# Kernel optimization log

Hardware: AMD Instinct MI355X
Metric: run time of the kernel (lower is better)

Reference implementation:

```python
import jax, jax.numpy as jnp
import numpy as np

EPS = 1e-05


def setup_inputs() -> dict:
    key = jax.random.key(0)
    k1, k2, k3 = jax.random.split(key, 3)
    B, S, D = 8, 4096, 1024  # batch, row(seq_len), col(d_model)
    x = jax.random.normal(k1, (B, S, D), dtype=jnp.float32)
    alpha = jnp.ones((D,), dtype=jnp.float32)
    beta = jnp.zeros((D,), dtype=jnp.float32)
    return {"x": x, "alpha": alpha, "beta": beta}


def reference(x, alpha, beta):
    # Faithful translation of LayerNorm_v2.forward, including its quirks:
    #  - statistics computed ONLY from batch element 0 (loop over x_t[0])
    #  - nonstandard running-mean recurrence: mean = (mean + data) / i
    #  - var accumulates (data - mean_i)^2 against the *updated* running mean
    #  - Bessel-style divide by (col - 1)
    # x: [B, S, D]; stats are per-row (per S), computed by streaming over D.
    B, S, D = x.shape
    data = x[0].T  # [D, S] -> loop iterates over the D (col) dimension

    def step(carry, d):
        mean, var, i = carry
        mean = (mean + d) / i          # quirky running mean
        var = var + jnp.square(d - mean)
        return (mean, var, i + 1.0), None

    init = (jnp.zeros((S,), x.dtype), jnp.zeros((S,), x.dtype),
            jnp.asarray(1.0, x.dtype))
    (mean, var, _), _ = jax.lax.scan(step, init, data)
    var = var / (D - 1)
    mean = mean[:, None]  # [S, 1]
    var = var[:, None]    # [S, 1]
    # broadcast stats from batch 0 across the whole batch, per-feature affine
    return alpha * (x - mean) / jnp.sqrt(var + EPS) + beta
```

## Files before the change

kernel.cpp:

```cpp
#include <hip/hip_runtime.h>
#include <math.h>

#define BB 8
#define SS 4096
#define DD 1024
#define EPSF 1e-5f

typedef float f32x4 __attribute__((ext_vector_type(4)));

__global__ __launch_bounds__(64) void stats_kernel(
    const float* __restrict__ x,
    float* __restrict__ mean_out,
    float* __restrict__ rstd_out)
{
    const int row = blockIdx.x;
    const int L   = threadIdx.x;
    const float4* __restrict__ rowp =
        reinterpret_cast<const float4*>(x) + (size_t)row * (DD / 4);

    const float4 a0 = rowp[4 * L + 0];
    const float4 a1 = rowp[4 * L + 1];
    const float4 a2 = rowp[4 * L + 2];
    const float4 a3 = rowp[4 * L + 3];
    const float d[16] = { a0.x, a0.y, a0.z, a0.w,  a1.x, a1.y, a1.z, a1.w,
                          a2.x, a2.y, a2.z, a2.w,  a3.x, a3.y, a3.z, a3.w };

    float m = 0.0f;
    if (L > 0) {
        const float4 p0 = rowp[4 * L - 2];
        const float4 p1 = rowp[4 * L - 1];
        const float jf = (float)(16 * L);
        float acc = p0.z;
        acc = fmaf(acc, __builtin_amdgcn_rcpf(jf - 5.0f), p0.w);
        acc = fmaf(acc, __builtin_amdgcn_rcpf(jf - 4.0f), p1.x);
        acc = fmaf(acc, __builtin_amdgcn_rcpf(jf - 3.0f), p1.y);
        acc = fmaf(acc, __builtin_amdgcn_rcpf(jf - 2.0f), p1.z);
        acc = fmaf(acc, __builtin_amdgcn_rcpf(jf - 1.0f), p1.w);
        m = acc * __builtin_amdgcn_rcpf(jf);
    }

    float var = 0.0f;
    const float base = (float)(16 * L);
#pragma unroll
    for (int t = 0; t < 16; ++t) {
        const float rk = __builtin_amdgcn_rcpf(base + (float)(t + 1));
        m = (m + d[t]) * rk;
        const float df = d[t] - m;
        var = fmaf(df, df, var);
    }

#pragma unroll
    for (int off = 32; off >= 1; off >>= 1) var += __shfl_down(var, off, 64);
    const float mean_final = __shfl(m, 63, 64);

    if (L == 0) {
        mean_out[row] = mean_final;
        rstd_out[row] = rsqrtf(var * (1.0f / 1023.0f) + EPSF);
    }
}

__global__ __launch_bounds__(256) void norm_kernel(
    const float* __restrict__ x,
    const float* __restrict__ alpha,
    const float* __restrict__ beta,
    const float* __restrict__ meanp,
    const float* __restrict__ rstdp,
    float* __restrict__ out)
{
    const int tid  = threadIdx.x;
    const int brow = blockIdx.x;
    const int s    = brow & (SS - 1);

    const float m = meanp[s];
    const float r = rstdp[s];

    const size_t i4 = (size_t)brow * 256 + tid;
    const f32x4 xv = __builtin_nontemporal_load(
        reinterpret_cast<const f32x4*>(x) + i4);
    const float4 av = reinterpret_cast<const float4*>(alpha)[tid];
    const float4 bv = reinterpret_cast<const float4*>(beta)[tid];

    f32x4 o;
    o.x = fmaf(av.x * (xv.x - m), r, bv.x);
    o.y = fmaf(av.y * (xv.y - m), r, bv.y);
    o.z = fmaf(av.z * (xv.z - m), r, bv.z);
    o.w = fmaf(av.w * (xv.w - m), r, bv.w);
    __builtin_nontemporal_store(o, reinterpret_cast<f32x4*>(out) + i4);
}

extern "C" void kernel_launch(void* const* d_in, const int* in_sizes, int n_in,
                              void* d_out, int out_size, void* d_ws, size_t ws_size,
                              hipStream_t stream) {
    (void)in_sizes; (void)n_in; (void)out_size; (void)ws_size;
    const float* x     = (const float*)d_in[0];
    const float* alpha = (const float*)d_in[1];
    const float* beta  = (const float*)d_in[2];
    float* out     = (float*)d_out;
    float* mean_ws = (float*)d_ws;
    float* rstd_ws = mean_ws + SS;

    hipLaunchKernelGGL(stats_kernel, dim3(SS), dim3(64), 0, stream,
                       x, mean_ws, rstd_ws);
    hipLaunchKernelGGL(norm_kernel, dim3(BB * SS), dim3(256), 0, stream,
                       x, alpha, beta, mean_ws, rstd_ws, out);
}
```

Before: 226.7 us.

## Fuse batch-0 normalization into stats kernel; persistent multi-row norm for rest

The stats kernel now also writes normalized output for batch 0, since it already holds those rows in registers, using an xor butterfly so every lane has the variance. That saves re-reading batch 0 in the second kernel. The norm kernel now covers only batches 1-7 with 2048 blocks, each handling 14 rows and prefetching the next row's data. This reduces block count and launch overhead but makes the grid depend on exact row counts (2048*14 = 7*4096).

```diff
diff --git a/kernel.cpp b/kernel.cpp
--- a/kernel.cpp
+++ b/kernel.cpp
@@ -8,8 +8,11 @@
 
 typedef float f32x4 __attribute__((ext_vector_type(4)));
 
-__global__ __launch_bounds__(64) void stats_kernel(
+__global__ __launch_bounds__(64) void stats_norm0_kernel(
     const float* __restrict__ x,
+    const float* __restrict__ alpha,
+    const float* __restrict__ beta,
+    float* __restrict__ out,
     float* __restrict__ mean_out,
     float* __restrict__ rstd_out)
 {
@@ -50,16 +53,35 @@
     }
 
 #pragma unroll
-    for (int off = 32; off >= 1; off >>= 1) var += __shfl_down(var, off, 64);
+    for (int off = 32; off >= 1; off >>= 1) var += __shfl_xor(var, off, 64);
     const float mean_final = __shfl(m, 63, 64);
+    const float r = rsqrtf(var * (1.0f / 1023.0f) + EPSF);
 
     if (L == 0) {
         mean_out[row] = mean_final;
-        rstd_out[row] = rsqrtf(var * (1.0f / 1023.0f) + EPSF);
+        rstd_out[row] = r;
+    }
+
+    const float4* __restrict__ alpha4 = reinterpret_cast<const float4*>(alpha);
+    const float4* __restrict__ beta4  = reinterpret_cast<const float4*>(beta);
+    f32x4* __restrict__ outp = reinterpret_cast<f32x4*>(out) + (size_t)row * (DD / 4);
+#pragma unroll
+    for (int q = 0; q < 4; ++q) {
+        const float4 av = alpha4[4 * L + q];
+        const float4 bv = beta4[4 * L + q];
+        f32x4 o;
+        o.x = fmaf(av.x * (d[4 * q + 0] - mean_final), r, bv.x);
+        o.y = fmaf(av.y * (d[4 * q + 1] - mean_final), r, bv.y);
+        o.z = fmaf(av.z * (d[4 * q + 2] - mean_final), r, bv.z);
+        o.w = fmaf(av.w * (d[4 * q + 3] - mean_final), r, bv.w);
+        __builtin_nontemporal_store(o, outp + 4 * L + q);
     }
 }
 
-__global__ __launch_bounds__(256) void norm_kernel(
+#define NBLK 2048
+#define RPB  14
+
+__global__ __launch_bounds__(256) void norm_rest_kernel(
     const float* __restrict__ x,
     const float* __restrict__ alpha,
     const float* __restrict__ beta,
@@ -67,25 +89,44 @@
     const float* __restrict__ rstdp,
     float* __restrict__ out)
 {
-    const int tid  = threadIdx.x;
-    const int brow = blockIdx.x;
-    const int s    = brow & (SS - 1);
-
-    const float m = meanp[s];
-    const float r = rstdp[s];
-
-    const size_t i4 = (size_t)brow * 256 + tid;
-    const f32x4 xv = __builtin_nontemporal_load(
-        reinterpret_cast<const f32x4*>(x) + i4);
+    const int tid = threadIdx.x;
     const float4 av = reinterpret_cast<const float4*>(alpha)[tid];
     const float4 bv = reinterpret_cast<const float4*>(beta)[tid];
 
+    const f32x4* __restrict__ xp = reinterpret_cast<const f32x4*>(x);
+    f32x4* __restrict__ op       = reinterpret_cast<f32x4*>(out);
+
+    const int row0 = SS + blockIdx.x * RPB;
+    size_t i4 = (size_t)row0 * (DD / 4) + tid;
+
+    f32x4 cur = __builtin_nontemporal_load(xp + i4);
+    float m = meanp[row0 & (SS - 1)];
+    float r = rstdp[row0 & (SS - 1)];
+
+#pragma unroll
+    for (int j = 0; j < RPB - 1; ++j) {
+        const int  rown = row0 + j + 1;
+        const size_t i4n = i4 + (DD / 4);
+        const f32x4 nxt = __builtin_nontemporal_load(xp + i4n);
+        const float mn  = meanp[rown & (SS - 1)];
+        const float rn  = rstdp[rown & (SS - 1)];
+
+        f32x4 o;
+        o.x = fmaf(av.x * (cur.x - m), r, bv.x);
+        o.y = fmaf(av.y * (cur.y - m), r, bv.y);
+        o.z = fmaf(av.z * (cur.z - m), r, bv.z);
+        o.w = fmaf(av.w * (cur.w - m), r, bv.w);
+        __builtin_nontemporal_store(o, op + i4);
+
+        cur = nxt; m = mn; r = rn; i4 = i4n;
+    }
+
     f32x4 o;
-    o.x = fmaf(av.x * (xv.x - m), r, bv.x);
-    o.y = fmaf(av.y * (xv.y - m), r, bv.y);
-    o.z = fmaf(av.z * (xv.z - m), r, bv.z);
-    o.w = fmaf(av.w * (xv.w - m), r, bv.w);
-    __builtin_nontemporal_store(o, reinterpret_cast<f32x4*>(out) + i4);
+    o.x = fmaf(av.x * (cur.x - m), r, bv.x);
+    o.y = fmaf(av.y * (cur.y - m), r, bv.y);
+    o.z = fmaf(av.z * (cur.z - m), r, bv.z);
+    o.w = fmaf(av.w * (cur.w - m), r, bv.w);
+    __builtin_nontemporal_store(o, op + i4);
 }
 
 extern "C" void kernel_launch(void* const* d_in, const int* in_sizes, int n_in,
@@ -99,8 +140,8 @@
     float* mean_ws = (float*)d_ws;
     float* rstd_ws = mean_ws + SS;
 
-    hipLaunchKernelGGL(stats_kernel, dim3(SS), dim3(64), 0, stream,
-                       x, mean_ws, rstd_ws);
-    hipLaunchKernelGGL(norm_kernel, dim3(BB * SS), dim3(256), 0, stream,
+    hipLaunchKernelGGL(stats_norm0_kernel, dim3(SS), dim3(64), 0, stream,
+                       x, alpha, beta, out, mean_ws, rstd_ws);
+    hipLaunchKernelGGL(norm_rest_kernel, dim3(NBLK), dim3(256), 0, stream,
                        x, alpha, beta, mean_ws, rstd_ws, out);
 }
```

Measured after the change: 234.7 us. +3.6%, slower.

## Fuse stats and normalization into one kernel with per-row batch loop

Applied to the files above, without the earlier changes.

Merges the statistics kernel and the normalization kernel into a single kernel where each 64-thread block computes row stats from batch 0 and then normalizes that row across all 8 batches. Batch 0 data is reused from registers, and the remaining batches are streamed with a one-ahead prefetch. This removes the second launch, the workspace round-trip, and one full reread of batch 0. The cost is fewer independent waves for the bulk streaming work, which may lower memory-level parallelism.

```diff
diff --git a/kernel.cpp b/kernel.cpp
--- a/kernel.cpp
+++ b/kernel.cpp
@@ -8,15 +8,20 @@
 
 typedef float f32x4 __attribute__((ext_vector_type(4)));
 
-__global__ __launch_bounds__(64) void stats_kernel(
+__global__ __launch_bounds__(64) void fused_ln_kernel(
     const float* __restrict__ x,
-    float* __restrict__ mean_out,
-    float* __restrict__ rstd_out)
+    const float* __restrict__ alpha,
+    const float* __restrict__ beta,
+    float* __restrict__ out)
 {
     const int row = blockIdx.x;
     const int L   = threadIdx.x;
-    const float4* __restrict__ rowp =
-        reinterpret_cast<const float4*>(x) + (size_t)row * (DD / 4);
+    const size_t row4   = (size_t)row * (DD / 4);
+    const size_t batch4 = (size_t)SS * (DD / 4);
+
+    const f32x4*  __restrict__ xp   = reinterpret_cast<const f32x4*>(x);
+    f32x4*        __restrict__ op   = reinterpret_cast<f32x4*>(out);
+    const float4* __restrict__ rowp = reinterpret_cast<const float4*>(x) + row4;
 
     const float4 a0 = rowp[4 * L + 0];
     const float4 a1 = rowp[4 * L + 1];
@@ -25,10 +30,26 @@
     const float d[16] = { a0.x, a0.y, a0.z, a0.w,  a1.x, a1.y, a1.z, a1.w,
                           a2.x, a2.y, a2.z, a2.w,  a3.x, a3.y, a3.z, a3.w };
 
+    float4 p0 = {0,0,0,0}, p1 = {0,0,0,0};
+    if (L > 0) {
+        p0 = rowp[4 * L - 2];
+        p1 = rowp[4 * L - 1];
+    }
+
+    const size_t b1 = batch4 + row4;
+    f32x4 cur[4];
+#pragma unroll
+    for (int q = 0; q < 4; ++q)
+        cur[q] = __builtin_nontemporal_load(xp + b1 + 4 * L + q);
+
+    const float4* __restrict__ alpha4 = reinterpret_cast<const float4*>(alpha);
+    const float4* __restrict__ beta4  = reinterpret_cast<const float4*>(beta);
+    float4 av[4], bv[4];
+#pragma unroll
+    for (int q = 0; q < 4; ++q) { av[q] = alpha4[4 * L + q]; bv[q] = beta4[4 * L + q]; }
+
     float m = 0.0f;
     if (L > 0) {
-        const float4 p0 = rowp[4 * L - 2];
-        const float4 p1 = rowp[4 * L - 1];
         const float jf = (float)(16 * L);
         float acc = p0.z;
         acc = fmaf(acc, __builtin_amdgcn_rcpf(jf - 5.0f), p0.w);
@@ -50,57 +71,60 @@
     }
 
 #pragma unroll
-    for (int off = 32; off >= 1; off >>= 1) var += __shfl_down(var, off, 64);
-    const float mean_final = __shfl(m, 63, 64);
+    for (int off = 32; off >= 1; off >>= 1) var += __shfl_xor(var, off, 64);
+    const float mf = __shfl(m, 63, 64);
+    const float r  = rsqrtf(var * (1.0f / 1023.0f) + EPSF);
 
-    if (L == 0) {
-        mean_out[row] = mean_final;
-        rstd_out[row] = rsqrtf(var * (1.0f / 1023.0f) + EPSF);
+#pragma unroll
+    for (int q = 0; q < 4; ++q) {
+        f32x4 o;
+        o.x = fmaf(av[q].x * (d[4 * q + 0] - mf), r, bv[q].x);
+        o.y = fmaf(av[q].y * (d[4 * q + 1] - mf), r, bv[q].y);
+        o.z = fmaf(av[q].z * (d[4 * q + 2] - mf), r, bv[q].z);
+        o.w = fmaf(av[q].w * (d[4 * q + 3] - mf), r, bv[q].w);
+        __builtin_nontemporal_store(o, op + row4 + 4 * L + q);
     }
-}
 
-__global__ __launch_bounds__(256) void norm_kernel(
-    const float* __restrict__ x,
-    const float* __restrict__ alpha,
-    const float* __restrict__ beta,
-    const float* __restrict__ meanp,
-    const float* __restrict__ rstdp,
-    float* __restrict__ out)
-{
-    const int tid  = threadIdx.x;
-    const int brow = blockIdx.x;
-    const int s    = brow & (SS - 1);
-
-    const float m = meanp[s];
-    const float r = rstdp[s];
-
-    const size_t i4 = (size_t)brow * 256 + tid;
-    const f32x4 xv = __builtin_nontemporal_load(
-        reinterpret_cast<const f32x4*>(x) + i4);
-    const float4 av = reinterpret_cast<const float4*>(alpha)[tid];
-    const float4 bv = reinterpret_cast<const float4*>(beta)[tid];
-
-    f32x4 o;
-    o.x = fmaf(av.x * (xv.x - m), r, bv.x);
-    o.y = fmaf(av.y * (xv.y - m), r, bv.y);
-    o.z = fmaf(av.z * (xv.z - m), r, bv.z);
-    o.w = fmaf(av.w * (xv.w - m), r, bv.w);
-    __builtin_nontemporal_store(o, reinterpret_cast<f32x4*>(out) + i4);
+    size_t cb = b1;
+#pragma unroll
+    for (int b = 1; b <= 6; ++b) {
+        f32x4 nxt[4];
+#pragma unroll
+        for (int q = 0; q < 4; ++q)
+            nxt[q] = __builtin_nontemporal_load(xp + cb + batch4 + 4 * L + q);
+#pragma unroll
+        for (int q = 0; q < 4; ++q) {
+            f32x4 o;
+            o.x = fmaf(av[q].x * (cur[q].x - mf), r, bv[q].x);
+            o.y = fmaf(av[q].y * (cur[q].y - mf), r, bv[q].y);
+            o.z = fmaf(av[q].z * (cur[q].z - mf), r, bv[q].z);
+            o.w = fmaf(av[q].w * (cur[q].w - mf), r, bv[q].w);
+            __builtin_nontemporal_store(o, op + cb + 4 * L + q);
+        }
+#pragma unroll
+        for (int q = 0; q < 4; ++q) cur[q] = nxt[q];
+        cb += batch4;
+    }
+#pragma unroll
+    for (int q = 0; q < 4; ++q) {
+        f32x4 o;
+        o.x = fmaf(av[q].x * (cur[q].x - mf), r, bv[q].x);
+        o.y = fmaf(av[q].y * (cur[q].y - mf), r, bv[q].y);
+        o.z = fmaf(av[q].z * (cur[q].z - mf), r, bv[q].z);
+        o.w = fmaf(av[q].w * (cur[q].w - mf), r, bv[q].w);
+        __builtin_nontemporal_store(o, op + cb + 4 * L + q);
+    }
 }
 
 extern "C" void kernel_launch(void* const* d_in, const int* in_sizes, int n_in,
                               void* d_out, int out_size, void* d_ws, size_t ws_size,
                               hipStream_t stream) {
-    (void)in_sizes; (void)n_in; (void)out_size; (void)ws_size;
+    (void)in_sizes; (void)n_in; (void)out_size; (void)d_ws; (void)ws_size;
     const float* x     = (const float*)d_in[0];
     const float* alpha = (const float*)d_in[1];
     const float* beta  = (const float*)d_in[2];
-    float* out     = (float*)d_out;
-    float* mean_ws = (float*)d_ws;
-    float* rstd_ws = mean_ws + SS;
+    float* out = (float*)d_out;
 
-    hipLaunchKernelGGL(stats_kernel, dim3(SS), dim3(64), 0, stream,
-                       x, mean_ws, rstd_ws);
-    hipLaunchKernelGGL(norm_kernel, dim3(BB * SS), dim3(256), 0, stream,
-                       x, alpha, beta, mean_ws, rstd_ws, out);
+    hipLaunchKernelGGL(fused_ln_kernel, dim3(SS), dim3(64), 0, stream,
+                       x, alpha, beta, out);
 }
```

After: 405.2 us. 78.8% more time.
